# Kernel tuning notes

Measured on AMD Instinct MI355X. Metric: run time of the kernel, lower is better.

The kernel has to match this reference:

```python
import jax, jax.numpy as jnp
import numpy as np

H = 128      # mamba_num_heads
P = 64       # mamba_head_dim
G = 8        # n_groups
N = 128      # ssm_state_size
CS = 128     # chunk_size
K = 4        # conv kernel size
DIM = 4096
INTER = H * P                 # 8192
CONV_DIM = INTER + 2 * G * N  # 10240
EPS = 1e-5


def segment_sum(x):
    # x: (..., T). Returns (..., T, T) with [i,j] = sum_{k=j+1..i} x[k] for i>=j, else -inf.
    T = x.shape[-1]
    x = jnp.repeat(x[..., None], T, axis=-1)
    x = jnp.where(jnp.tril(jnp.ones((T, T), dtype=bool), -1), x, 0.0)
    s = jnp.cumsum(x, axis=-2)
    return jnp.where(jnp.tril(jnp.ones((T, T), dtype=bool), 0), s, -jnp.inf)


def setup_inputs() -> dict:
    key = jax.random.key(0)
    ks = jax.random.split(key, 8)
    Bz, L = 1, 2048
    return {
        "hidden_states": jax.random.normal(ks[0], (Bz, L, DIM), jnp.float32),
        "in_proj_w": jax.random.normal(ks[1], (INTER + CONV_DIM + H, DIM), jnp.float32) * 0.02,
        "conv_w": jax.random.normal(ks[2], (CONV_DIM, 1, K), jnp.float32) * 0.2,
        "conv_b": jnp.zeros((CONV_DIM,), jnp.float32),
        "dt_bias": jnp.log(jnp.exp(jnp.linspace(0.001, 0.1, H)) - 1.0).astype(jnp.float32),
        "A_log": jnp.log(jax.random.uniform(ks[3], (H,), jnp.float32, 1.0, 16.0)),
        "D": jnp.ones((H,), jnp.float32),
        "norm_w": jnp.ones((INTER,), jnp.float32),
        "out_proj_w": jax.random.normal(ks[4], (DIM, INTER), jnp.float32) * 0.02,
    }


def reference(hidden_states, in_proj_w, conv_w, conv_b, dt_bias, A_log, D, norm_w, out_proj_w):
    Bz, L, _ = hidden_states.shape
    proj = hidden_states @ in_proj_w.T  # (B,L,INTER+CONV_DIM+H)
    gate = proj[..., :INTER]
    hBC = proj[..., INTER:INTER + CONV_DIM]
    dt = proj[..., INTER + CONV_DIM:]

    # causal depthwise conv1d + silu
    xc = jnp.transpose(hBC, (0, 2, 1))  # (B, CONV_DIM, L)
    xc = jax.lax.conv_general_dilated(
        xc, conv_w, (1,), [(K - 1, 0)],
        dimension_numbers=("NCH", "OIH", "NCH"),
        feature_group_count=CONV_DIM) + conv_b[None, :, None]
    hBC = jax.nn.silu(jnp.transpose(xc, (0, 2, 1)))

    x = hBC[..., :INTER].reshape(Bz, L, H, P)
    Bm = hBC[..., INTER:INTER + G * N].reshape(Bz, L, G, N)
    Cm = hBC[..., INTER + G * N:].reshape(Bz, L, G, N)
    Bm = jnp.repeat(Bm, H // G, axis=2)  # (B,L,H,N)
    Cm = jnp.repeat(Cm, H // G, axis=2)

    dt = jax.nn.softplus(dt + dt_bias)  # (B,L,H); dt_limit=(0,inf) -> no clamp
    A = -jnp.exp(A_log)                 # (H,)

    D_residual = D[None, None, :, None] * x
    A_dt = A[None, None, :] * dt        # (B,L,H)
    x_dt = x * dt[..., None]

    Cn = L // CS  # L chosen divisible by chunk_size (pad_size = 0)
    Ac = jnp.transpose(A_dt.reshape(Bz, Cn, CS, H), (0, 3, 1, 2))  # (B,H,Cn,CS)
    xch = x_dt.reshape(Bz, Cn, CS, H, P)
    Bch = Bm.reshape(Bz, Cn, CS, H, N)
    Cch = Cm.reshape(Bz, Cn, CS, H, N)

    A_cumsum = jnp.cumsum(Ac, axis=-1)
    Lmat = jnp.exp(segment_sum(Ac))  # (B,H,Cn,CS,CS)

    # 1. intra-chunk diagonal block outputs
    Gm = jnp.einsum("bclhn,bcshn->bclsh", Cch, Bch)
    M = Gm * jnp.transpose(Lmat, (0, 2, 3, 4, 1))
    Y_diag = jnp.einsum("bclsh,bcshp->bclhp", M, xch)

    # 2. per-chunk end states
    decay_states = jnp.exp(A_cumsum[..., -1:] - A_cumsum)  # (B,H,Cn,CS)
    B_decay = Bch * jnp.transpose(decay_states, (0, 2, 3, 1))[..., None]
    states = jnp.einsum("bclhn,bclhp->bchpn", B_decay, xch)

    # 3. inter-chunk recurrence via segment_sum over chunk decays
    states_cat = jnp.concatenate([jnp.zeros_like(states[:, :1]), states], axis=1)  # (B,Cn+1,H,P,N)
    A_last = jnp.pad(A_cumsum[..., -1], ((0, 0), (0, 0), (1, 0)))
    decay_chunk = jnp.exp(segment_sum(A_last))  # (B,H,Cn+1,Cn+1)
    new_states = jnp.einsum("bhij,bjhpn->bihpn", decay_chunk, states_cat)
    states = new_states[:, :-1]  # (B,Cn,H,P,N)

    # 4. state -> output conversion
    state_decay = jnp.transpose(jnp.exp(A_cumsum), (0, 2, 3, 1))  # (B,Cn,CS,H)
    Y_off = jnp.einsum("bclhn,bchpn->bclhp", Cch, states) * state_decay[..., None]

    y = (Y_diag + Y_off).reshape(Bz, L, H, P) + D_residual
    y = y.reshape(Bz, L, INTER)

    # gated RMSNorm (computed in fp32)
    var = jnp.mean(jnp.square(y), axis=-1, keepdims=True)
    y = y * jax.lax.rsqrt(var + EPS) * norm_w
    y = y * jax.nn.silu(gate)

    return y @ out_proj_w.T
```

## Files before the change

kernel.cpp:

```cpp
#include <hip/hip_runtime.h>
#include <hip/hip_bf16.h>

#define L_    2048
#define DIM_  4096
#define H_    128
#define P_    64
#define G_    8
#define NST_  128
#define CS_   128
#define NC_   16
#define INTER_ 8192
#define CONVD_ 10240
#define NPROJ_ 18560

typedef unsigned short u16;
typedef __attribute__((ext_vector_type(8))) __bf16 bf16x8;
typedef __attribute__((ext_vector_type(4))) float f32x4;

__device__ __forceinline__ u16 f2bf(float f) {
  unsigned u = __float_as_uint(f);
  u += 0x7FFFu + ((u >> 16) & 1u);
  return (u16)(u >> 16);
}
__device__ __forceinline__ float bf2f(u16 v) {
  return __uint_as_float(((unsigned)v) << 16);
}
__device__ __forceinline__ float silu_f(float x) {
  return x / (1.f + expf(-x));
}

__device__ __forceinline__ f32x4 mfma_bf16(bf16x8 a, bf16x8 b, f32x4 c) {
  return __builtin_amdgcn_mfma_f32_16x16x32_bf16(a, b, c, 0, 0, 0);
}

__global__ __launch_bounds__(256) void cast_k(const float* __restrict__ src,
                                              u16* __restrict__ dst, int n4) {
  int i = blockIdx.x * 256 + threadIdx.x;
  if (i >= n4) return;
  float4 v = ((const float4*)src)[i];
  ushort4 o = make_ushort4(f2bf(v.x), f2bf(v.y), f2bf(v.z), f2bf(v.w));
  ((ushort4*)dst)[i] = o;
}

__global__ __launch_bounds__(256) void gemm_bt(const u16* __restrict__ A,
                                               const u16* __restrict__ B,
                                               float* __restrict__ C,
                                               int M, int N, int K) {
  __shared__ __align__(16) u16 sA[128 * 40];
  __shared__ __align__(16) u16 sB[128 * 40];
  const int tid = threadIdx.x;
  const int lane = tid & 63, wv = tid >> 6;
  const int lr = lane & 15, kg = lane >> 4;
  const int wm = (wv >> 1) << 6, wn = (wv & 1) << 6;
  const int bm = blockIdx.x << 7, bn = blockIdx.y << 7;
  const int r0 = tid >> 2, cg = tid & 3;

  const u16* Ap = A + (size_t)(bm + r0) * K + cg * 8;
  const u16* Bp = B + (size_t)(bn + r0) * K + cg * 8;

  f32x4 acc[4][4] = {};
  for (int k0 = 0; k0 < K; k0 += 32) {
    __syncthreads();
    *(int4*)&sA[r0 * 40 + cg * 8]        = *(const int4*)(Ap + k0);
    *(int4*)&sA[(r0 + 64) * 40 + cg * 8] = *(const int4*)(Ap + (size_t)64 * K + k0);
    *(int4*)&sB[r0 * 40 + cg * 8]        = *(const int4*)(Bp + k0);
    *(int4*)&sB[(r0 + 64) * 40 + cg * 8] = *(const int4*)(Bp + (size_t)64 * K + k0);
    __syncthreads();
    bf16x8 av[4], bv[4];
#pragma unroll
    for (int mi = 0; mi < 4; ++mi) av[mi] = *(const bf16x8*)&sA[(wm + mi * 16 + lr) * 40 + kg * 8];
#pragma unroll
    for (int ni = 0; ni < 4; ++ni) bv[ni] = *(const bf16x8*)&sB[(wn + ni * 16 + lr) * 40 + kg * 8];
#pragma unroll
    for (int mi = 0; mi < 4; ++mi)
#pragma unroll
      for (int ni = 0; ni < 4; ++ni)
        acc[mi][ni] = mfma_bf16(av[mi], bv[ni], acc[mi][ni]);
  }
#pragma unroll
  for (int mi = 0; mi < 4; ++mi)
#pragma unroll
    for (int ni = 0; ni < 4; ++ni) {
      f32x4 a4 = acc[mi][ni];
#pragma unroll
      for (int r = 0; r < 4; ++r) {
        int row = bm + wm + mi * 16 + kg * 4 + r;
        int col = bn + wn + ni * 16 + lr;
        C[(size_t)row * N + col] = a4[r];
      }
    }
}

__global__ __launch_bounds__(256) void conv_silu(const float* __restrict__ proj,
                                                 const float* __restrict__ cw,
                                                 const float* __restrict__ cb,
                                                 u16* __restrict__ xo,
                                                 u16* __restrict__ Bo,
                                                 u16* __restrict__ Co) {
  int ci = blockIdx.x * 256 + threadIdx.x;
  int l = blockIdx.y;
  const float* w = cw + ci * 4;
  float a = cb[ci];
#pragma unroll
  for (int k = 0; k < 4; ++k) {
    int ls = l - 3 + k;
    if (ls >= 0) a += proj[(size_t)ls * NPROJ_ + INTER_ + ci] * w[k];
  }
  u16 bv = f2bf(silu_f(a));
  if (ci < INTER_)             xo[(size_t)l * INTER_ + ci] = bv;
  else if (ci < INTER_ + 1024) Bo[(size_t)l * 1024 + (ci - INTER_)] = bv;
  else                         Co[(size_t)l * 1024 + (ci - INTER_ - 1024)] = bv;
}

__global__ __launch_bounds__(256) void dt_k(const float* __restrict__ proj,
                                            const float* __restrict__ dt_bias,
                                            float* __restrict__ dtb) {
  int i = blockIdx.x * 256 + threadIdx.x;
  int l = i >> 7, h = i & 127;
  float z = proj[(size_t)l * NPROJ_ + (INTER_ + CONVD_) + h] + dt_bias[h];
  dtb[i] = (z > 20.f) ? z : log1pf(expf(z));
}

__global__ __launch_bounds__(256) void ssm_intra(const u16* __restrict__ xb,
                                                 const u16* __restrict__ Bb,
                                                 const u16* __restrict__ Cb,
                                                 const float* __restrict__ dtb,
                                                 const float* __restrict__ A_log,
                                                 const float* __restrict__ Dp,
                                                 float* __restrict__ acum_g,
                                                 float* __restrict__ states,
                                                 float* __restrict__ Y) {
  __shared__ __align__(16) u16 bufM[128 * 136];
  __shared__ __align__(16) u16 buf3[64 * 136];
  __shared__ float s_dt[128];
  __shared__ float s_ac[128];
  const int c = blockIdx.x, h = blockIdx.y, g = h >> 4;
  const int tid = threadIdx.x;
  const int lane = tid & 63, wv = tid >> 6;
  const int lr = lane & 15, kg = lane >> 4;

  float Ah = -expf(A_log[h]);
  if (tid < 128) {
    float dv = dtb[(size_t)(c * 128 + tid) * 128 + h];
    s_dt[tid] = dv;
    s_ac[tid] = Ah * dv;
  }
  __syncthreads();
  for (int off = 1; off < 128; off <<= 1) {
    float v = 0.f;
    if (tid < 128 && tid >= off) v = s_ac[tid - off];
    __syncthreads();
    if (tid < 128) s_ac[tid] += v;
    __syncthreads();
  }
  if (tid < 128) acum_g[((size_t)c * 128 + h) * 128 + tid] = s_ac[tid];

  for (int it = 0; it < 32; ++it) {
    int idx = tid + 256 * it;
    int p = idx & 63, srow = idx >> 6;
    float xv = bf2f(xb[(size_t)(c * 128 + srow) * INTER_ + h * 64 + p]);
    buf3[p * 136 + srow] = f2bf(xv * s_dt[srow]);
  }

  const u16* Cbase = Cb + (size_t)c * 128 * 1024 + g * 128;
  const u16* Bbase = Bb + (size_t)c * 128 * 1024 + g * 128;
  const int wm = (wv >> 1) << 6, wn = (wv & 1) << 6;
  f32x4 S[4][4] = {};
  for (int ks = 0; ks < 128; ks += 32) {
    bf16x8 av[4], bv[4];
#pragma unroll
    for (int mi = 0; mi < 4; ++mi)
      av[mi] = *(const bf16x8*)(Cbase + (size_t)(wm + mi * 16 + lr) * 1024 + ks + kg * 8);
#pragma unroll
    for (int ni = 0; ni < 4; ++ni)
      bv[ni] = *(const bf16x8*)(Bbase + (size_t)(wn + ni * 16 + lr) * 1024 + ks + kg * 8);
#pragma unroll
    for (int mi = 0; mi < 4; ++mi)
#pragma unroll
      for (int ni = 0; ni < 4; ++ni)
        S[mi][ni] = mfma_bf16(av[mi], bv[ni], S[mi][ni]);
  }

#pragma unroll
  for (int mi = 0; mi < 4; ++mi)
#pragma unroll
    for (int ni = 0; ni < 4; ++ni) {
      f32x4 sv = S[mi][ni];
#pragma unroll
      for (int r = 0; r < 4; ++r) {
        int l = wm + mi * 16 + kg * 4 + r;
        int s = wn + ni * 16 + lr;
        float mv = 0.f;
        if (l >= s) mv = sv[r] * expf(s_ac[l] - s_ac[s]);
        bufM[l * 136 + s] = f2bf(mv);
      }
    }
  __syncthreads();

  f32x4 yacc[2][4] = {};
  for (int ks = 0; ks < 128; ks += 32) {
    bf16x8 am[2], bx[4];
#pragma unroll
    for (int mi = 0; mi < 2; ++mi)
      am[mi] = *(const bf16x8*)&bufM[(32 * wv + mi * 16 + lr) * 136 + ks + kg * 8];
#pragma unroll
    for (int ni = 0; ni < 4; ++ni)
      bx[ni] = *(const bf16x8*)&buf3[(ni * 16 + lr) * 136 + ks + kg * 8];
#pragma unroll
    for (int mi = 0; mi < 2; ++mi)
#pragma unroll
      for (int ni = 0; ni < 4; ++ni)
        yacc[mi][ni] = mfma_bf16(am[mi], bx[ni], yacc[mi][ni]);
  }
  float Dh = Dp[h];
#pragma unroll
  for (int mi = 0; mi < 2; ++mi)
#pragma unroll
    for (int ni = 0; ni < 4; ++ni) {
      f32x4 yv = yacc[mi][ni];
#pragma unroll
      for (int r = 0; r < 4; ++r) {
        int l = 32 * wv + mi * 16 + kg * 4 + r;
        int p = ni * 16 + lr;
        size_t o = (size_t)(c * 128 + l) * INTER_ + h * 64 + p;
        Y[o] = yv[r] + Dh * bf2f(xb[o]);
      }
    }

  float aclast = s_ac[127];
  __syncthreads();
  for (int it = 0; it < 64; ++it) {
    int idx = tid + 256 * it;
    int n = idx & 127, lrow = idx >> 7;
    float bvv = bf2f(Bb[(size_t)(c * 128 + lrow) * 1024 + g * 128 + n]);
    bufM[n * 136 + lrow] = f2bf(bvv * expf(aclast - s_ac[lrow]));
  }
  __syncthreads();
  f32x4 st[8] = {};
  for (int ks = 0; ks < 128; ks += 32) {
    bf16x8 ax = *(const bf16x8*)&buf3[(16 * wv + lr) * 136 + ks + kg * 8];
#pragma unroll
    for (int ni = 0; ni < 8; ++ni) {
      bf16x8 bn = *(const bf16x8*)&bufM[(ni * 16 + lr) * 136 + ks + kg * 8];
      st[ni] = mfma_bf16(ax, bn, st[ni]);
    }
  }
#pragma unroll
  for (int ni = 0; ni < 8; ++ni) {
    f32x4 sv = st[ni];
#pragma unroll
    for (int r = 0; r < 4; ++r) {
      int p = 16 * wv + kg * 4 + r;
      int n = ni * 16 + lr;
      states[(((size_t)c * 128 + h) * 64 + p) * 128 + n] = sv[r];
    }
  }
}

__global__ __launch_bounds__(256) void scan_k(float* __restrict__ states,
                                              const float* __restrict__ acum_g) {
  int j = blockIdx.x * 256 + threadIdx.x;
  int h = j >> 13;
  float run = 0.f;
  float* p = states + j;
  for (int c = 0; c < NC_; ++c) {
    float dk = expf(acum_g[((size_t)c * 128 + h) * 128 + 127]);
    float v = p[(size_t)c * 1048576];
    p[(size_t)c * 1048576] = run;
    run = run * dk + v;
  }
}

__global__ __launch_bounds__(256) void ssm_off(const u16* __restrict__ Cb,
                                               const float* __restrict__ states,
                                               const float* __restrict__ acum_g,
                                               float* __restrict__ Y) {
  const int c = blockIdx.x, h = blockIdx.y, g = h >> 4;
  const int tid = threadIdx.x, lane = tid & 63, wv = tid >> 6;
  const int lr = lane & 15, kg = lane >> 4;
  const u16* Cbase = Cb + (size_t)c * 128 * 1024 + g * 128;
  const float* sbase = states + ((size_t)c * 128 + h) * 64 * 128;
  f32x4 acc[2][4] = {};
  for (int ks = 0; ks < 128; ks += 32) {
    bf16x8 av[2], bv[4];
#pragma unroll
    for (int mi = 0; mi < 2; ++mi)
      av[mi] = *(const bf16x8*)(Cbase + (size_t)(32 * wv + mi * 16 + lr) * 1024 + ks + kg * 8);
#pragma unroll
    for (int ni = 0; ni < 4; ++ni) {
      const float* sp = sbase + (size_t)(ni * 16 + lr) * 128 + ks + kg * 8;
      float4 u0 = *(const float4*)sp;
      float4 u1 = *(const float4*)(sp + 4);
      union { bf16x8 v; u16 u[8]; } t;
      t.u[0] = f2bf(u0.x); t.u[1] = f2bf(u0.y); t.u[2] = f2bf(u0.z); t.u[3] = f2bf(u0.w);
      t.u[4] = f2bf(u1.x); t.u[5] = f2bf(u1.y); t.u[6] = f2bf(u1.z); t.u[7] = f2bf(u1.w);
      bv[ni] = t.v;
    }
#pragma unroll
    for (int mi = 0; mi < 2; ++mi)
#pragma unroll
      for (int ni = 0; ni < 4; ++ni)
        acc[mi][ni] = mfma_bf16(av[mi], bv[ni], acc[mi][ni]);
  }
  const float* ac = acum_g + ((size_t)c * 128 + h) * 128;
#pragma unroll
  for (int mi = 0; mi < 2; ++mi)
#pragma unroll
    for (int ni = 0; ni < 4; ++ni) {
      f32x4 a4 = acc[mi][ni];
#pragma unroll
      for (int r = 0; r < 4; ++r) {
        int l = 32 * wv + mi * 16 + kg * 4 + r;
        int p = ni * 16 + lr;
        size_t o = (size_t)(c * 128 + l) * INTER_ + h * 64 + p;
        Y[o] += expf(ac[l]) * a4[r];
      }
    }
}

__global__ __launch_bounds__(256) void norm_gate(const float* __restrict__ Y,
                                                 const float* __restrict__ proj,
                                                 const float* __restrict__ norm_w,
                                                 u16* __restrict__ ybf) {
  const int l = blockIdx.x, tid = threadIdx.x;
  const float* yr = Y + (size_t)l * INTER_;
  float ss = 0.f;
  for (int i = tid; i < 2048; i += 256) {
    float4 v = ((const float4*)yr)[i];
    ss += v.x * v.x + v.y * v.y + v.z * v.z + v.w * v.w;
  }
  for (int off = 32; off > 0; off >>= 1) ss += __shfl_down(ss, off, 64);
  __shared__ float red[4];
  if ((tid & 63) == 0) red[tid >> 6] = ss;
  __syncthreads();
  float rs = rsqrtf((red[0] + red[1] + red[2] + red[3]) * (1.f / 8192.f) + 1e-5f);
  const float* gr = proj + (size_t)l * NPROJ_;
  for (int i = tid; i < 2048; i += 256) {
    float4 v = ((const float4*)yr)[i];
    float4 gv = ((const float4*)gr)[i];
    float4 nw = ((const float4*)norm_w)[i];
    ushort4 o = make_ushort4(f2bf(v.x * rs * nw.x * silu_f(gv.x)),
                             f2bf(v.y * rs * nw.y * silu_f(gv.y)),
                             f2bf(v.z * rs * nw.z * silu_f(gv.z)),
                             f2bf(v.w * rs * nw.w * silu_f(gv.w)));
    ((ushort4*)ybf)[(size_t)l * 2048 + i] = o;
  }
}

extern "C" void kernel_launch(void* const* d_in, const int* in_sizes, int n_in,
                              void* d_out, int out_size, void* d_ws, size_t ws_size,
                              hipStream_t stream) {
  const float* hs      = (const float*)d_in[0];
  const float* w_in    = (const float*)d_in[1];
  const float* conv_w  = (const float*)d_in[2];
  const float* conv_b  = (const float*)d_in[3];
  const float* dt_bias = (const float*)d_in[4];
  const float* A_log   = (const float*)d_in[5];
  const float* Dv      = (const float*)d_in[6];
  const float* norm_w  = (const float*)d_in[7];
  const float* w_out   = (const float*)d_in[8];
  float* out = (float*)d_out;

  char* ws = (char*)d_ws;
  u16*   hs_bf   = (u16*)(ws + 0);
  u16*   win_bf  = (u16*)(ws + 16777216);
  float* states  = (float*)(ws + 16777216);
  float* Yb      = (float*)(ws + 16777216 + 67108864);
  float* proj    = (float*)(ws + 168820736);
  u16*   wout_bf = (u16*)(ws + 168820736);
  u16*   xb      = (u16*)(ws + 320864256);
  u16*   ybf     = (u16*)(ws + 320864256);
  u16*   Bb      = (u16*)(ws + 354418688);
  u16*   Cbuf    = (u16*)(ws + 358612992);
  float* dtb     = (float*)(ws + 362807296);
  float* acum    = (float*)(ws + 363855872);

  cast_k<<<(L_ * DIM_ / 4 + 255) / 256, 256, 0, stream>>>(hs, hs_bf, L_ * DIM_ / 4);
  cast_k<<<(NPROJ_ * DIM_ / 4 + 255) / 256, 256, 0, stream>>>(w_in, win_bf, NPROJ_ * DIM_ / 4);
  gemm_bt<<<dim3(L_ / 128, NPROJ_ / 128), 256, 0, stream>>>(hs_bf, win_bf, proj, L_, NPROJ_, DIM_);
  conv_silu<<<dim3(CONVD_ / 256, L_), 256, 0, stream>>>(proj, conv_w, conv_b, xb, Bb, Cbuf);
  dt_k<<<(L_ * H_) / 256, 256, 0, stream>>>(proj, dt_bias, dtb);
  ssm_intra<<<dim3(NC_, H_), 256, 0, stream>>>(xb, Bb, Cbuf, dtb, A_log, Dv, acum, states, Yb);
  scan_k<<<(H_ * P_ * NST_) / 256, 256, 0, stream>>>(states, acum);
  ssm_off<<<dim3(NC_, H_), 256, 0, stream>>>(Cbuf, states, acum, Yb);
  norm_gate<<<L_, 256, 0, stream>>>(Yb, proj, norm_w, ybf);
  cast_k<<<(DIM_ * INTER_ / 4 + 255) / 256, 256, 0, stream>>>(w_out, wout_bf, DIM_ * INTER_ / 4);
  gemm_bt<<<dim3(L_ / 128, DIM_ / 128), 256, 0, stream>>>(ybf, wout_bf, out, L_, DIM_, INTER_);
}
```

Baseline: 1.574 ms.

## Rewrite GEMMs with large tiles, direct-to-LDS loads and a 4-stage pipeline

Replaces the simple 128x128 single-buffered bf16 GEMM with a templated 512-thread kernel using 256x256 or 128x256 tiles. Operands stream through four LDS stages via global_load_lds with XOR-swizzled layout, explicit vmcnt waits and barriers, and MFMA priority raising. An XCD-aware block remap is applied to the in-projection. The aim is to hide global-load latency, raise data reuse per block and avoid bank conflicts. The cost is heavy LDS use (up to 128KB), which limits occupancy. The last column tile of the in-projection reads weight rows past N, and only the stores are guarded.

Result: faster. 1.390 ms (-11.7%).

```diff
diff --git a/kernel.cpp b/kernel.cpp
--- a/kernel.cpp
+++ b/kernel.cpp
@@ -33,6 +33,14 @@
   return __builtin_amdgcn_mfma_f32_16x16x32_bf16(a, b, c, 0, 0, 0);
 }
 
+__device__ __forceinline__ void glds16(const u16* g, u16* l) {
+  const auto* gp = (const __attribute__((address_space(1))) unsigned int*)(unsigned long long)(g);
+  auto* lp = (__attribute__((address_space(3))) unsigned int*)(unsigned long long)(l);
+  __builtin_amdgcn_global_load_lds(gp, lp, 16, 0, 0);
+}
+
+#define S_BARRIER() asm volatile("s_barrier" ::: "memory")
+
 __global__ __launch_bounds__(256) void cast_k(const float* __restrict__ src,
                                               u16* __restrict__ dst, int n4) {
   int i = blockIdx.x * 256 + threadIdx.x;
@@ -42,51 +50,138 @@
   ((ushort4*)dst)[i] = o;
 }
 
-__global__ __launch_bounds__(256) void gemm_bt(const u16* __restrict__ A,
-                                               const u16* __restrict__ B,
-                                               float* __restrict__ C,
-                                               int M, int N, int K) {
-  __shared__ __align__(16) u16 sA[128 * 40];
-  __shared__ __align__(16) u16 sB[128 * 40];
+template <int MI, int SWZ>
+__global__ __launch_bounds__(512) void gemm_p(const u16* __restrict__ A,
+                                              const u16* __restrict__ B,
+                                              float* __restrict__ C,
+                                              int M, int N, int K, int nbm) {
+  constexpr int BM = MI * 32;
+  constexpr int ATILE2 = BM * 32;
+  constexpr int BTILE2 = 256 * 32;
+  constexpr int TILE2 = ATILE2 + BTILE2;
+  constexpr int AJ = BM / 128;
+  __shared__ __align__(16) u16 lds[4 * TILE2];
+
   const int tid = threadIdx.x;
   const int lane = tid & 63, wv = tid >> 6;
+  const int wvm = wv >> 2, wvn = wv & 3;
   const int lr = lane & 15, kg = lane >> 4;
-  const int wm = (wv >> 1) << 6, wn = (wv & 1) << 6;
-  const int bm = blockIdx.x << 7, bn = blockIdx.y << 7;
-  const int r0 = tid >> 2, cg = tid & 3;
-
-  const u16* Ap = A + (size_t)(bm + r0) * K + cg * 8;
-  const u16* Bp = B + (size_t)(bn + r0) * K + cg * 8;
-
-  f32x4 acc[4][4] = {};
-  for (int k0 = 0; k0 < K; k0 += 32) {
-    __syncthreads();
-    *(int4*)&sA[r0 * 40 + cg * 8]        = *(const int4*)(Ap + k0);
-    *(int4*)&sA[(r0 + 64) * 40 + cg * 8] = *(const int4*)(Ap + (size_t)64 * K + k0);
-    *(int4*)&sB[r0 * 40 + cg * 8]        = *(const int4*)(Bp + k0);
-    *(int4*)&sB[(r0 + 64) * 40 + cg * 8] = *(const int4*)(Bp + (size_t)64 * K + k0);
-    __syncthreads();
+  const int cofs = ((kg * 16) ^ ((lr << 3) & 0x30)) >> 1;
+
+  int lin = blockIdx.x;
+  if (SWZ) { const int ch = gridDim.x >> 3; lin = (lin & 7) * ch + (lin >> 3); }
+  const int bm = (lin % nbm) * BM;
+  const int bn = (lin / nbm) * 256;
+
+  const u16* gA[2];
+  const u16* gB[2];
+  int dA[2], dB[2];
+#pragma unroll
+  for (int j = 0; j < AJ; ++j) {
+    int o = (j * 512 + tid) * 16;
+    int b = o ^ ((o >> 3) & 0x30);
+    gA[j] = A + (size_t)(bm + (b >> 6)) * K + ((b & 63) >> 1);
+    dA[j] = o >> 1;
+  }
+#pragma unroll
+  for (int j = 0; j < 2; ++j) {
+    int o = (j * 512 + tid) * 16;
+    int b = o ^ ((o >> 3) & 0x30);
+    gB[j] = B + (size_t)(bn + (b >> 6)) * K + ((b & 63) >> 1);
+    dB[j] = ATILE2 + (o >> 1);
+  }
+
+  const int NT = K >> 5;
+  f32x4 acc[MI][4] = {};
+
+#pragma unroll
+  for (int tt = 0; tt < 3; ++tt) {
+#pragma unroll
+    for (int j = 0; j < AJ; ++j) glds16(gA[j] + tt * 32, &lds[tt * TILE2 + dA[j]]);
+#pragma unroll
+    for (int j = 0; j < 2; ++j)  glds16(gB[j] + tt * 32, &lds[tt * TILE2 + dB[j]]);
+  }
+  if constexpr (AJ == 2) { asm volatile("s_waitcnt vmcnt(8)" ::: "memory"); }
+  else                   { asm volatile("s_waitcnt vmcnt(6)" ::: "memory"); }
+  S_BARRIER();
+
+  for (int t = 0; t < NT; ++t) {
+    const int rb = (t & 3) * TILE2;
+    const int sb = ((t + 3) & 3) * TILE2;
+    const bool st = (t + 3 < NT);
+    const int abase = rb + (wvm * (MI * 16) + lr) * 32 + cofs;
+    const int bbase = rb + ATILE2 + (wvn * 64 + lr) * 32 + cofs;
+
     bf16x8 av[4], bv[4];
 #pragma unroll
-    for (int mi = 0; mi < 4; ++mi) av[mi] = *(const bf16x8*)&sA[(wm + mi * 16 + lr) * 40 + kg * 8];
-#pragma unroll
-    for (int ni = 0; ni < 4; ++ni) bv[ni] = *(const bf16x8*)&sB[(wn + ni * 16 + lr) * 40 + kg * 8];
-#pragma unroll
-    for (int mi = 0; mi < 4; ++mi)
-#pragma unroll
-      for (int ni = 0; ni < 4; ++ni)
-        acc[mi][ni] = mfma_bf16(av[mi], bv[ni], acc[mi][ni]);
-  }
-#pragma unroll
-  for (int mi = 0; mi < 4; ++mi)
+    for (int mi = 0; mi < 4; ++mi) av[mi] = *(const bf16x8*)&lds[abase + mi * 512];
+#pragma unroll
+    for (int ni = 0; ni < 4; ++ni) bv[ni] = *(const bf16x8*)&lds[bbase + ni * 512];
+
+    if constexpr (MI == 8) {
+      if (st) {
+#pragma unroll
+        for (int j = 0; j < 2; ++j) glds16(gA[j] + (t + 3) * 32, &lds[sb + dA[j]]);
+      }
+      S_BARRIER();
+      __builtin_amdgcn_s_setprio(1);
+#pragma unroll
+      for (int mi = 0; mi < 4; ++mi)
+#pragma unroll
+        for (int ni = 0; ni < 4; ++ni)
+          acc[mi][ni] = mfma_bf16(av[mi], bv[ni], acc[mi][ni]);
+      __builtin_amdgcn_s_setprio(0);
+      S_BARRIER();
+      bf16x8 aw[4];
+#pragma unroll
+      for (int mi = 0; mi < 4; ++mi) aw[mi] = *(const bf16x8*)&lds[abase + (mi + 4) * 512];
+      if (st) {
+#pragma unroll
+        for (int j = 0; j < 2; ++j) glds16(gB[j] + (t + 3) * 32, &lds[sb + dB[j]]);
+      }
+      S_BARRIER();
+      __builtin_amdgcn_s_setprio(1);
+#pragma unroll
+      for (int mi = 0; mi < 4; ++mi)
+#pragma unroll
+        for (int ni = 0; ni < 4; ++ni)
+          acc[mi + 4][ni] = mfma_bf16(aw[mi], bv[ni], acc[mi + 4][ni]);
+      __builtin_amdgcn_s_setprio(0);
+      if (st)              { asm volatile("s_waitcnt vmcnt(8)" ::: "memory"); }
+      else if (t + 2 < NT) { asm volatile("s_waitcnt vmcnt(4)" ::: "memory"); }
+      else if (t + 1 < NT) { asm volatile("s_waitcnt vmcnt(0)" ::: "memory"); }
+      S_BARRIER();
+    } else {
+      if (st) {
+        glds16(gA[0] + (t + 3) * 32, &lds[sb + dA[0]]);
+#pragma unroll
+        for (int j = 0; j < 2; ++j) glds16(gB[j] + (t + 3) * 32, &lds[sb + dB[j]]);
+      }
+      S_BARRIER();
+      __builtin_amdgcn_s_setprio(1);
+#pragma unroll
+      for (int mi = 0; mi < 4; ++mi)
+#pragma unroll
+        for (int ni = 0; ni < 4; ++ni)
+          acc[mi][ni] = mfma_bf16(av[mi], bv[ni], acc[mi][ni]);
+      __builtin_amdgcn_s_setprio(0);
+      if (st)              { asm volatile("s_waitcnt vmcnt(6)" ::: "memory"); }
+      else if (t + 2 < NT) { asm volatile("s_waitcnt vmcnt(3)" ::: "memory"); }
+      else if (t + 1 < NT) { asm volatile("s_waitcnt vmcnt(0)" ::: "memory"); }
+      S_BARRIER();
+    }
+  }
+
+#pragma unroll
+  for (int mi = 0; mi < MI; ++mi)
 #pragma unroll
     for (int ni = 0; ni < 4; ++ni) {
       f32x4 a4 = acc[mi][ni];
 #pragma unroll
       for (int r = 0; r < 4; ++r) {
-        int row = bm + wm + mi * 16 + kg * 4 + r;
-        int col = bn + wn + ni * 16 + lr;
-        C[(size_t)row * N + col] = a4[r];
+        int row = bm + wvm * (MI * 16) + mi * 16 + kg * 4 + r;
+        int col = bn + wvn * 64 + ni * 16 + lr;
+        if (col < N) C[(size_t)row * N + col] = a4[r];
       }
     }
 }
@@ -377,7 +472,7 @@
 
   cast_k<<<(L_ * DIM_ / 4 + 255) / 256, 256, 0, stream>>>(hs, hs_bf, L_ * DIM_ / 4);
   cast_k<<<(NPROJ_ * DIM_ / 4 + 255) / 256, 256, 0, stream>>>(w_in, win_bf, NPROJ_ * DIM_ / 4);
-  gemm_bt<<<dim3(L_ / 128, NPROJ_ / 128), 256, 0, stream>>>(hs_bf, win_bf, proj, L_, NPROJ_, DIM_);
+  gemm_p<8, 1><<<dim3(8 * 73), 512, 0, stream>>>(hs_bf, win_bf, proj, L_, NPROJ_, DIM_, 8);
   conv_silu<<<dim3(CONVD_ / 256, L_), 256, 0, stream>>>(proj, conv_w, conv_b, xb, Bb, Cbuf);
   dt_k<<<(L_ * H_) / 256, 256, 0, stream>>>(proj, dt_bias, dtb);
   ssm_intra<<<dim3(NC_, H_), 256, 0, stream>>>(xb, Bb, Cbuf, dtb, A_log, Dv, acum, states, Yb);
@@ -385,5 +480,5 @@
   ssm_off<<<dim3(NC_, H_), 256, 0, stream>>>(Cbuf, states, acum, Yb);
   norm_gate<<<L_, 256, 0, stream>>>(Yb, proj, norm_w, ybf);
   cast_k<<<(DIM_ * INTER_ / 4 + 255) / 256, 256, 0, stream>>>(w_out, wout_bf, DIM_ * INTER_ / 4);
-  gemm_bt<<<dim3(L_ / 128, DIM_ / 128), 256, 0, stream>>>(ybf, wout_bf, out, L_, DIM_, INTER_);
-}
+  gemm_p<4, 0><<<dim3(16 * 16), 512, 0, stream>>>(ybf, wout_bf, out, L_, DIM_, INTER_, 16);
+}
```
